# Kernel tuning notes

Hardware: AMD Instinct MI355X
Metric: run time of the kernel (lower is better)

## Reference

```python
import jax, jax.numpy as jnp
import numpy as np

OUT_LEN = 25  # fixed self.out_length
H1, H2, D_IN, D_OUT = 9, 32, 5, 3


def _rnn_last(x_tbd, Wih, Whh, b):
    """Elman tanh RNN, time-major input [T,B,D]; returns final hidden [B,H]."""
    B = x_tbd.shape[1]
    h0 = jnp.zeros((B, Wih.shape[0]), x_tbd.dtype)
    def step(h, x_t):
        h = jnp.tanh(x_t @ Wih.T + h @ Whh.T + b)
        return h, None
    h_last, _ = jax.lax.scan(step, h0, x_tbd)
    return h_last


def _rnn_all(x_tbd, Wih, Whh, b):
    """Elman tanh RNN, time-major input [T,B,D]; returns all hiddens [T,B,H]."""
    B = x_tbd.shape[1]
    h0 = jnp.zeros((B, Wih.shape[0]), x_tbd.dtype)
    def step(h, x_t):
        h = jnp.tanh(x_t @ Wih.T + h @ Whh.T + b)
        return h, h
    _, hs = jax.lax.scan(step, h0, x_tbd)
    return hs


def setup_inputs() -> dict:
    key = jax.random.key(0)
    ks = jax.random.split(key, 16)
    B, T = 4096, 2048
    s1 = 1.0 / np.sqrt(H1)
    s2 = 1.0 / np.sqrt(H2)
    u = lambda k, shp, s: jax.random.uniform(k, shp, jnp.float32, -s, s)
    return {
        "x": jax.random.uniform(ks[0], (B, T, D_IN), jnp.float32),
        # rnn_1 forward direction
        "w_ih_f": u(ks[1], (H1, D_IN), s1), "w_hh_f": u(ks[2], (H1, H1), s1),
        "b_ih_f": u(ks[3], (H1,), s1),     "b_hh_f": u(ks[4], (H1,), s1),
        # rnn_1 backward direction
        "w_ih_b": u(ks[5], (H1, D_IN), s1), "w_hh_b": u(ks[6], (H1, H1), s1),
        "b_ih_b": u(ks[7], (H1,), s1),      "b_hh_b": u(ks[8], (H1,), s1),
        # rnn_2 (input 2*H1=18, hidden 32)
        "w_ih2": u(ks[9], (H2, 2 * H1), s2), "w_hh2": u(ks[10], (H2, H2), s2),
        "b_ih2": u(ks[11], (H2,), s2),       "b_hh2": u(ks[12], (H2,), s2),
        # output linear 32 -> 3
        "w_out": u(ks[13], (D_OUT, H2), s2), "b_out": u(ks[14], (D_OUT,), s2),
    }


def reference(x, w_ih_f, w_hh_f, b_ih_f, b_hh_f,
              w_ih_b, w_hh_b, b_ih_b, b_hh_b,
              w_ih2, w_hh2, b_ih2, b_hh2, w_out, b_out):
    B = x.shape[0]
    xt = jnp.swapaxes(x, 0, 1)  # [T,B,5]
    h_f = _rnn_last(xt, w_ih_f, w_hh_f, b_ih_f + b_hh_f)          # [B,9]
    h_b = _rnn_last(xt[::-1], w_ih_b, w_hh_b, b_ih_b + b_hh_b)    # [B,9]
    y = jnp.concatenate([h_f, h_b], axis=1)                       # [B,18]
    # u: zeros over OUT_LEN steps with y at t=0 (time-major)
    u = jnp.zeros((OUT_LEN, B, 2 * H1), x.dtype).at[0].set(y)
    ys = _rnn_all(u, w_ih2, w_hh2, b_ih2 + b_hh2)                 # [25,B,32]
    ys = jnp.swapaxes(ys, 0, 1)                                   # [B,25,32]
    out = jnp.einsum('bth,oh->bto', ys, w_out) + b_out            # [B,25,3]
    return out
```

## Files before the change

kernel.cpp:

```cpp
#include <hip/hip_runtime.h>

#define RNN_T 2048
#define RNN_B 4096
#define BLK 16
#define NBLK (RNN_T / BLK)
#define CHF (BLK * 5)
#define WVF (4 * CHF)
#define BLF (16 * CHF)

__device__ __forceinline__ void async4(const float* src, float* dst) {
    __builtin_amdgcn_global_load_lds(
        (const __attribute__((address_space(1))) void*)src,
        (__attribute__((address_space(3))) void*)dst, 4, 0, 0);
}

__device__ __forceinline__ void fill_wave(float* dstWave, const float* x,
                                          unsigned (&off)[5], int adv) {
#pragma unroll
    for (int j = 0; j < 5; ++j) {
        async4(x + off[j], dstWave + j * 64);
        off[j] += (unsigned)adv;
    }
}

__device__ __forceinline__ void stepr(float& h, float xn, const float (&W)[16],
                                      float bb, bool own) {
    float a0 = fmaf(h, W[0], bb);
    float a1, a2;
    asm ("s_nop 1\n\t"
         "v_fmac_f32_dpp %0, %3, %4  row_ror:1  row_mask:0xf bank_mask:0xf\n\t"
         "v_mul_f32_dpp  %1, %3, %5  row_ror:2  row_mask:0xf bank_mask:0xf\n\t"
         "v_mul_f32_dpp  %2, %3, %6  row_ror:3  row_mask:0xf bank_mask:0xf\n\t"
         "v_fmac_f32_dpp %0, %3, %7  row_ror:4  row_mask:0xf bank_mask:0xf\n\t"
         "v_fmac_f32_dpp %1, %3, %8  row_ror:5  row_mask:0xf bank_mask:0xf\n\t"
         "v_fmac_f32_dpp %2, %3, %9  row_ror:6  row_mask:0xf bank_mask:0xf\n\t"
         "v_fmac_f32_dpp %0, %3, %10 row_ror:7  row_mask:0xf bank_mask:0xf\n\t"
         "v_fmac_f32_dpp %1, %3, %11 row_ror:8  row_mask:0xf bank_mask:0xf\n\t"
         "v_fmac_f32_dpp %2, %3, %12 row_ror:9  row_mask:0xf bank_mask:0xf\n\t"
         "v_fmac_f32_dpp %0, %3, %13 row_ror:10 row_mask:0xf bank_mask:0xf\n\t"
         "v_fmac_f32_dpp %1, %3, %14 row_ror:11 row_mask:0xf bank_mask:0xf\n\t"
         "v_fmac_f32_dpp %2, %3, %15 row_ror:12 row_mask:0xf bank_mask:0xf\n\t"
         "v_fmac_f32_dpp %0, %3, %16 row_ror:13 row_mask:0xf bank_mask:0xf\n\t"
         "v_fmac_f32_dpp %1, %3, %17 row_ror:14 row_mask:0xf bank_mask:0xf\n\t"
         "v_fmac_f32_dpp %2, %3, %18 row_ror:15 row_mask:0xf bank_mask:0xf"
         : "+v"(a0), "=&v"(a1), "=&v"(a2)
         : "v"(h), "v"(W[1]), "v"(W[2]), "v"(W[3]), "v"(W[4]), "v"(W[5]),
           "v"(W[6]), "v"(W[7]), "v"(W[8]), "v"(W[9]), "v"(W[10]), "v"(W[11]),
           "v"(W[12]), "v"(W[13]), "v"(W[14]), "v"(W[15]));
    const float z = (a0 + a1) + a2;
    const float e = __builtin_amdgcn_exp2f(z);
    const float u = __builtin_amdgcn_rcpf(e + 1.0f);
    h = own ? u : xn;
}

template <bool FWD, bool FILL>
__device__ __forceinline__ void compute_block(const float* xc, const float* xnb,
        float& h, const float (&W)[16], float bb, bool own,
        float* fillDst, const float* x, unsigned (&off)[5], int adv) {
    float xn[16];
#pragma unroll
    for (int j = 0; j < 15; ++j) xn[j] = xc[FWD ? (j + 1) * 5 : (14 - j) * 5];
    xn[15] = xnb[FWD ? 0 : 75];
    if constexpr (FILL) fill_wave(fillDst, x, off, adv);
#pragma unroll
    for (int j = 0; j < 16; ++j) stepr(h, xn[j], W, bb, own);
}

template <bool FWD>
__device__ __forceinline__ float run_all(const float* xcA, const float* xcB,
        const float* xcC, float* wA, float* wB, float* wC,
        const float* x, unsigned (&off)[5], int adv,
        const float (&W)[16], float bb, bool own) {
    fill_wave(wA, x, off, adv);
    fill_wave(wB, x, off, adv);
    float h = own ? 0.5f : xcA[FWD ? 0 : 75];
#pragma unroll 1
    for (int it = 0; it < 42; ++it) {
        compute_block<FWD, true >(xcA, xcB, h, W, bb, own, wC, x, off, adv);
        compute_block<FWD, true >(xcB, xcC, h, W, bb, own, wA, x, off, adv);
        compute_block<FWD, true >(xcC, xcA, h, W, bb, own, wB, x, off, adv);
    }
    compute_block<FWD, false>(xcA, xcB, h, W, bb, own, wC, x, off, adv);
    compute_block<FWD, false>(xcB, xcB, h, W, bb, own, wC, x, off, adv);
    return h;
}

__global__ __launch_bounds__(256, 2) void rnn1_kernel(
    const float* __restrict__ x,
    const float* __restrict__ w_ih_f, const float* __restrict__ w_hh_f,
    const float* __restrict__ b_ih_f, const float* __restrict__ b_hh_f,
    const float* __restrict__ w_ih_b, const float* __restrict__ w_hh_b,
    const float* __restrict__ b_ih_b, const float* __restrict__ b_hh_b,
    float* __restrict__ y)
{
    __shared__ __align__(16) float sA[BLF], sB[BLF], sC[BLF];
    const float SC = 2.8853900817779268f;
    const int tid    = threadIdx.x;
    const int group  = tid >> 4;
    const int lane16 = tid & 15;
    const int waveId = tid >> 6;
    const int lane   = tid & 63;
    const int chain  = blockIdx.x * 16 + group;
    const int b      = chain & (RNN_B - 1);
    const int dir    = chain >> 12;

    const float* __restrict__ wih = dir ? w_ih_b : w_ih_f;
    const float* __restrict__ whh = dir ? w_hh_b : w_hh_f;
    const float* __restrict__ bih = dir ? b_ih_b : b_ih_f;
    const float* __restrict__ bhh = dir ? b_hh_b : b_hh_f;

    const int   li  = (lane16 < 9) ? lane16 : 0;
    const float msk = (lane16 < 9) ? SC : 0.0f;
    const bool  own = (lane16 < 9);
    float W[16];
    float wsum = 0.0f;
#pragma unroll
    for (int r = 0; r < 16; ++r) {
        const int s = (lane16 - r) & 15;
        float w = 0.0f;
        bool hs = false;
        if (s < 9)       { w = whh[li * 9 + s]; hs = true; }
        else if (s < 14) w = wih[li * 5 + (s - 9)];
        w *= msk;
        if (hs) { wsum += w; w *= -2.0f; }
        W[r] = w;
    }
    const float bb = (bih[li] + bhh[li]) * msk + wsum;

    unsigned off[5];
#pragma unroll
    for (int j = 0; j < 5; ++j) {
        const int idx = j * 64 + lane;
        const int gf  = idx / 80;
        const int p   = idx - gf * 80;
        const int bf  = (blockIdx.x * 16 + waveId * 4 + gf) & (RNN_B - 1);
        off[j] = (unsigned)(bf * (RNN_T * 5) + (dir ? (NBLK - 1) * CHF : 0) + p);
    }
    const int adv = dir ? -CHF : CHF;

    float* wA = sA + waveId * WVF;
    float* wB = sB + waveId * WVF;
    float* wC = sC + waveId * WVF;
    const int xoff = own ? 0 : ((lane16 < 14) ? (lane16 - 9) : 0);
    const float* xcA = sA + group * CHF + xoff;
    const float* xcB = sB + group * CHF + xoff;
    const float* xcC = sC + group * CHF + xoff;

    float h = dir ? run_all<false>(xcA, xcB, xcC, wA, wB, wC, x, off, adv, W, bb, own)
                  : run_all<true >(xcA, xcB, xcC, wA, wB, wC, x, off, adv, W, bb, own);

    if (lane16 < 9) y[b * 18 + dir * 9 + lane16] = fmaf(-2.0f, h, 1.0f);
}

__global__ __launch_bounds__(256) void rnn2_kernel(
    const float* __restrict__ y,
    const float* __restrict__ w_ih2, const float* __restrict__ w_hh2,
    const float* __restrict__ b_ih2, const float* __restrict__ b_hh2,
    const float* __restrict__ w_out, const float* __restrict__ b_out,
    float* __restrict__ out)
{
    __shared__ float hist[8][25][32];
    const float SC = 2.8853900817779268f;
    const int bl = threadIdx.x >> 5;
    const int i  = threadIdx.x & 31;
    const int b  = blockIdx.x * 8 + bl;

    float wr[32];
#pragma unroll
    for (int k = 0; k < 32; ++k) wr[k] = w_hh2[i * 32 + k] * SC;
    const float bias = (b_ih2[i] + b_hh2[i]) * SC;

    const float* yb = y + b * 18;
    float z = bias;
#pragma unroll
    for (int k = 0; k < 18; ++k) z = fmaf(w_ih2[i * 18 + k] * SC, yb[k], z);
    {
        float e = __builtin_amdgcn_exp2f(z);
        float r = __builtin_amdgcn_rcpf(e + 1.0f);
        hist[bl][0][i] = fmaf(-2.0f, r, 1.0f);
    }
    __syncthreads();

    for (int t = 1; t < 25; ++t) {
        float zz = bias;
#pragma unroll
        for (int k = 0; k < 32; ++k) zz = fmaf(wr[k], hist[bl][t - 1][k], zz);
        float e = __builtin_amdgcn_exp2f(zz);
        float r = __builtin_amdgcn_rcpf(e + 1.0f);
        hist[bl][t][i] = fmaf(-2.0f, r, 1.0f);
        __syncthreads();
    }

    for (int e = threadIdx.x; e < 600; e += 256) {
        const int o  = e % 3;
        const int t  = (e / 3) % 25;
        const int b2 = e / 75;
        float acc = b_out[o];
#pragma unroll
        for (int k = 0; k < 32; ++k) acc = fmaf(w_out[o * 32 + k], hist[b2][t][k], acc);
        out[((size_t)(blockIdx.x * 8 + b2) * 25 + t) * 3 + o] = acc;
    }
}

extern "C" void kernel_launch(void* const* d_in, const int* in_sizes, int n_in,
                              void* d_out, int out_size, void* d_ws, size_t ws_size,
                              hipStream_t stream) {
    const float* x      = (const float*)d_in[0];
    const float* w_ih_f = (const float*)d_in[1];
    const float* w_hh_f = (const float*)d_in[2];
    const float* b_ih_f = (const float*)d_in[3];
    const float* b_hh_f = (const float*)d_in[4];
    const float* w_ih_b = (const float*)d_in[5];
    const float* w_hh_b = (const float*)d_in[6];
    const float* b_ih_b = (const float*)d_in[7];
    const float* b_hh_b = (const float*)d_in[8];
    const float* w_ih2  = (const float*)d_in[9];
    const float* w_hh2  = (const float*)d_in[10];
    const float* b_ih2  = (const float*)d_in[11];
    const float* b_hh2  = (const float*)d_in[12];
    const float* w_out  = (const float*)d_in[13];
    const float* b_out  = (const float*)d_in[14];

    float* y = (float*)d_ws;

    rnn1_kernel<<<dim3(512), dim3(256), 0, stream>>>(
        x, w_ih_f, w_hh_f, b_ih_f, b_hh_f,
        w_ih_b, w_hh_b, b_ih_b, b_hh_b, y);

    rnn2_kernel<<<dim3(RNN_B / 8), dim3(256), 0, stream>>>(
        y, w_ih2, w_hh2, b_ih2, b_hh2, w_out, b_out, (float*)d_out);
}
```

Measured before the change: 418.1 us.

## Interleave two independent RNN chains per lane group to hide transcendental latency

```diff
diff --git a/kernel.cpp b/kernel.cpp
--- a/kernel.cpp
+++ b/kernel.cpp
@@ -5,8 +5,8 @@
 #define BLK 16
 #define NBLK (RNN_T / BLK)
 #define CHF (BLK * 5)
-#define WVF (4 * CHF)
-#define BLF (16 * CHF)
+#define WVF (8 * CHF)
+#define BLF (32 * CHF)
 
 __device__ __forceinline__ void async4(const float* src, float* dst) {
     __builtin_amdgcn_global_load_lds(
@@ -15,16 +15,16 @@
 }
 
 __device__ __forceinline__ void fill_wave(float* dstWave, const float* x,
-                                          unsigned (&off)[5], int adv) {
-#pragma unroll
-    for (int j = 0; j < 5; ++j) {
+                                          unsigned (&off)[10], int adv) {
+#pragma unroll
+    for (int j = 0; j < 10; ++j) {
         async4(x + off[j], dstWave + j * 64);
         off[j] += (unsigned)adv;
     }
 }
 
-__device__ __forceinline__ void stepr(float& h, float xn, const float (&W)[16],
-                                      float bb, bool own) {
+__device__ __forceinline__ void mac16(float h, const float (&W)[16], float bb,
+                                      float& a0o, float& a1o, float& a2o) {
     float a0 = fmaf(h, W[0], bb);
     float a1, a2;
     asm ("s_nop 1\n\t"
@@ -47,45 +47,62 @@
          : "v"(h), "v"(W[1]), "v"(W[2]), "v"(W[3]), "v"(W[4]), "v"(W[5]),
            "v"(W[6]), "v"(W[7]), "v"(W[8]), "v"(W[9]), "v"(W[10]), "v"(W[11]),
            "v"(W[12]), "v"(W[13]), "v"(W[14]), "v"(W[15]));
-    const float z = (a0 + a1) + a2;
-    const float e = __builtin_amdgcn_exp2f(z);
-    const float u = __builtin_amdgcn_rcpf(e + 1.0f);
-    h = own ? u : xn;
+    a0o = a0; a1o = a1; a2o = a2;
 }
 
 template <bool FWD, bool FILL>
-__device__ __forceinline__ void compute_block(const float* xc, const float* xnb,
-        float& h, const float (&W)[16], float bb, bool own,
-        float* fillDst, const float* x, unsigned (&off)[5], int adv) {
-    float xn[16];
-#pragma unroll
-    for (int j = 0; j < 15; ++j) xn[j] = xc[FWD ? (j + 1) * 5 : (14 - j) * 5];
-    xn[15] = xnb[FWD ? 0 : 75];
+__device__ __forceinline__ void compute_block2(const float* xcA, const float* xcAn,
+        const float* xcB, const float* xcBn,
+        float& hA, float& hB, const float (&W)[16], float bb, bool own,
+        float* fillDst, const float* x, unsigned (&off)[10], int adv) {
+    float xnA[16], xnB[16];
+#pragma unroll
+    for (int j = 0; j < 15; ++j) {
+        xnA[j] = xcA[FWD ? (j + 1) * 5 : (14 - j) * 5];
+        xnB[j] = xcB[FWD ? (j + 1) * 5 : (14 - j) * 5];
+    }
+    xnA[15] = xcAn[FWD ? 0 : 75];
+    xnB[15] = xcBn[FWD ? 0 : 75];
     if constexpr (FILL) fill_wave(fillDst, x, off, adv);
-#pragma unroll
-    for (int j = 0; j < 16; ++j) stepr(h, xn[j], W, bb, own);
+
+    float a0, a1, a2, b0, b1, b2, eA, eB;
+    mac16(hA, W, bb, a0, a1, a2);
+    eA = __builtin_amdgcn_exp2f((a0 + a1) + a2);
+    mac16(hB, W, bb, b0, b1, b2);
+    { float u = __builtin_amdgcn_rcpf(eA + 1.0f); hA = own ? u : xnA[0]; }
+    eB = __builtin_amdgcn_exp2f((b0 + b1) + b2);
+#pragma unroll
+    for (int j = 1; j < 16; ++j) {
+        mac16(hA, W, bb, a0, a1, a2);
+        { float u = __builtin_amdgcn_rcpf(eB + 1.0f); hB = own ? u : xnB[j - 1]; }
+        eA = __builtin_amdgcn_exp2f((a0 + a1) + a2);
+        mac16(hB, W, bb, b0, b1, b2);
+        { float u = __builtin_amdgcn_rcpf(eA + 1.0f); hA = own ? u : xnA[j]; }
+        eB = __builtin_amdgcn_exp2f((b0 + b1) + b2);
+    }
+    { float u = __builtin_amdgcn_rcpf(eB + 1.0f); hB = own ? u : xnB[15]; }
 }
 
 template <bool FWD>
-__device__ __forceinline__ float run_all(const float* xcA, const float* xcB,
-        const float* xcC, float* wA, float* wB, float* wC,
-        const float* x, unsigned (&off)[5], int adv,
-        const float (&W)[16], float bb, bool own) {
+__device__ __forceinline__ void run_all2(const float* pA, const float* pB,
+        const float* pC, float* wA, float* wB, float* wC,
+        const float* x, unsigned (&off)[10], int adv,
+        const float (&W)[16], float bb, bool own, float& hA, float& hB) {
     fill_wave(wA, x, off, adv);
     fill_wave(wB, x, off, adv);
-    float h = own ? 0.5f : xcA[FWD ? 0 : 75];
+    hA = own ? 0.5f : pA[FWD ? 0 : 75];
+    hB = own ? 0.5f : pA[320 + (FWD ? 0 : 75)];
 #pragma unroll 1
     for (int it = 0; it < 42; ++it) {
-        compute_block<FWD, true >(xcA, xcB, h, W, bb, own, wC, x, off, adv);
-        compute_block<FWD, true >(xcB, xcC, h, W, bb, own, wA, x, off, adv);
-        compute_block<FWD, true >(xcC, xcA, h, W, bb, own, wB, x, off, adv);
-    }
-    compute_block<FWD, false>(xcA, xcB, h, W, bb, own, wC, x, off, adv);
-    compute_block<FWD, false>(xcB, xcB, h, W, bb, own, wC, x, off, adv);
-    return h;
-}
-
-__global__ __launch_bounds__(256, 2) void rnn1_kernel(
+        compute_block2<FWD, true >(pA, pB, pA + 320, pB + 320, hA, hB, W, bb, own, wC, x, off, adv);
+        compute_block2<FWD, true >(pB, pC, pB + 320, pC + 320, hA, hB, W, bb, own, wA, x, off, adv);
+        compute_block2<FWD, true >(pC, pA, pC + 320, pA + 320, hA, hB, W, bb, own, wB, x, off, adv);
+    }
+    compute_block2<FWD, false>(pA, pB, pA + 320, pB + 320, hA, hB, W, bb, own, wC, x, off, adv);
+    compute_block2<FWD, false>(pB, pB, pB + 320, pB + 320, hA, hB, W, bb, own, wC, x, off, adv);
+}
+
+__global__ __launch_bounds__(256, 1) void rnn1_kernel(
     const float* __restrict__ x,
     const float* __restrict__ w_ih_f, const float* __restrict__ w_hh_f,
     const float* __restrict__ b_ih_f, const float* __restrict__ b_hh_f,
@@ -100,9 +117,9 @@
     const int lane16 = tid & 15;
     const int waveId = tid >> 6;
     const int lane   = tid & 63;
-    const int chain  = blockIdx.x * 16 + group;
-    const int b      = chain & (RNN_B - 1);
-    const int dir    = chain >> 12;
+    const int slot   = blockIdx.x * 16 + group;
+    const int dir    = (slot >= 2048) ? 1 : 0;
+    const int bA     = slot - (dir ? 2048 : 0);
 
     const float* __restrict__ wih = dir ? w_ih_b : w_ih_f;
     const float* __restrict__ whh = dir ? w_hh_b : w_hh_f;
@@ -127,13 +144,14 @@
     }
     const float bb = (bih[li] + bhh[li]) * msk + wsum;
 
-    unsigned off[5];
-#pragma unroll
-    for (int j = 0; j < 5; ++j) {
+    unsigned off[10];
+#pragma unroll
+    for (int j = 0; j < 10; ++j) {
         const int idx = j * 64 + lane;
         const int gf  = idx / 80;
         const int p   = idx - gf * 80;
-        const int bf  = (blockIdx.x * 16 + waveId * 4 + gf) & (RNN_B - 1);
+        const int slotf = blockIdx.x * 16 + waveId * 4 + (gf & 3);
+        const int bf  = (slotf - (dir ? 2048 : 0)) + ((gf >= 4) ? 2048 : 0);
         off[j] = (unsigned)(bf * (RNN_T * 5) + (dir ? (NBLK - 1) * CHF : 0) + p);
     }
     const int adv = dir ? -CHF : CHF;
@@ -141,15 +159,20 @@
     float* wA = sA + waveId * WVF;
     float* wB = sB + waveId * WVF;
     float* wC = sC + waveId * WVF;
-    const int xoff = own ? 0 : ((lane16 < 14) ? (lane16 - 9) : 0);
-    const float* xcA = sA + group * CHF + xoff;
-    const float* xcB = sB + group * CHF + xoff;
-    const float* xcC = sC + group * CHF + xoff;
-
-    float h = dir ? run_all<false>(xcA, xcB, xcC, wA, wB, wC, x, off, adv, W, bb, own)
-                  : run_all<true >(xcA, xcB, xcC, wA, wB, wC, x, off, adv, W, bb, own);
-
-    if (lane16 < 9) y[b * 18 + dir * 9 + lane16] = fmaf(-2.0f, h, 1.0f);
+    const int xoff  = own ? 0 : ((lane16 < 14) ? (lane16 - 9) : 0);
+    const int gbase = waveId * WVF + (group & 3) * CHF + xoff;
+    const float* pA = sA + gbase;
+    const float* pB = sB + gbase;
+    const float* pC = sC + gbase;
+
+    float hA, hB;
+    if (dir) run_all2<false>(pA, pB, pC, wA, wB, wC, x, off, adv, W, bb, own, hA, hB);
+    else     run_all2<true >(pA, pB, pC, wA, wB, wC, x, off, adv, W, bb, own, hA, hB);
+
+    if (lane16 < 9) {
+        y[bA * 18 + dir * 9 + lane16]          = fmaf(-2.0f, hA, 1.0f);
+        y[(bA + 2048) * 18 + dir * 9 + lane16] = fmaf(-2.0f, hB, 1.0f);
+    }
 }
 
 __global__ __launch_bounds__(256) void rnn2_kernel(
@@ -223,7 +246,7 @@
 
     float* y = (float*)d_ws;
 
-    rnn1_kernel<<<dim3(512), dim3(256), 0, stream>>>(
+    rnn1_kernel<<<dim3(256), dim3(256), 0, stream>>>(
         x, w_ih_f, w_hh_f, b_ih_f, b_hh_f,
         w_ih_b, w_hh_b, b_ih_b, b_hh_b, y);
 
```

New measurement: 482.0 us. +15.3%, slower.

## Double time chunk and transpose LDS staging for vectorized float4 reads

Applied to the files above, without the earlier changes.

```diff
diff --git a/kernel.cpp b/kernel.cpp
--- a/kernel.cpp
+++ b/kernel.cpp
@@ -2,7 +2,7 @@
 
 #define RNN_T 2048
 #define RNN_B 4096
-#define BLK 16
+#define BLK 32
 #define NBLK (RNN_T / BLK)
 #define CHF (BLK * 5)
 #define WVF (4 * CHF)
@@ -15,9 +15,9 @@
 }
 
 __device__ __forceinline__ void fill_wave(float* dstWave, const float* x,
-                                          unsigned (&off)[5], int adv) {
-#pragma unroll
-    for (int j = 0; j < 5; ++j) {
+                                          unsigned (&off)[10], int adv) {
+#pragma unroll
+    for (int j = 0; j < 10; ++j) {
         async4(x + off[j], dstWave + j * 64);
         off[j] += (unsigned)adv;
     }
@@ -54,34 +54,43 @@
 }
 
 template <bool FWD, bool FILL>
-__device__ __forceinline__ void compute_block(const float* xc, const float* xnb,
+__device__ __forceinline__ void compute_block(const float* xc,
         float& h, const float (&W)[16], float bb, bool own,
-        float* fillDst, const float* x, unsigned (&off)[5], int adv) {
-    float xn[16];
-#pragma unroll
-    for (int j = 0; j < 15; ++j) xn[j] = xc[FWD ? (j + 1) * 5 : (14 - j) * 5];
-    xn[15] = xnb[FWD ? 0 : 75];
+        float* fillDst, const float* x, unsigned (&off)[10], int adv) {
+    float xn[32];
+#pragma unroll
+    for (int j = 0; j < 8; ++j) {
+        const float4 v = *reinterpret_cast<const float4*>(xc + j * 4);
+        xn[j * 4 + 0] = v.x; xn[j * 4 + 1] = v.y;
+        xn[j * 4 + 2] = v.z; xn[j * 4 + 3] = v.w;
+    }
+    h = own ? h : xn[FWD ? 0 : 31];
     if constexpr (FILL) fill_wave(fillDst, x, off, adv);
 #pragma unroll
-    for (int j = 0; j < 16; ++j) stepr(h, xn[j], W, bb, own);
+    for (int j = 0; j < 32; ++j) {
+        const int nidx = FWD ? (j < 31 ? j + 1 : 31) : (j < 31 ? 30 - j : 0);
+        stepr(h, xn[nidx], W, bb, own);
+    }
 }
 
 template <bool FWD>
 __device__ __forceinline__ float run_all(const float* xcA, const float* xcB,
         const float* xcC, float* wA, float* wB, float* wC,
-        const float* x, unsigned (&off)[5], int adv,
+        const float* x, unsigned (&off)[10], int adv,
         const float (&W)[16], float bb, bool own) {
     fill_wave(wA, x, off, adv);
     fill_wave(wB, x, off, adv);
-    float h = own ? 0.5f : xcA[FWD ? 0 : 75];
+    float h = own ? 0.5f : 0.0f;
 #pragma unroll 1
-    for (int it = 0; it < 42; ++it) {
-        compute_block<FWD, true >(xcA, xcB, h, W, bb, own, wC, x, off, adv);
-        compute_block<FWD, true >(xcB, xcC, h, W, bb, own, wA, x, off, adv);
-        compute_block<FWD, true >(xcC, xcA, h, W, bb, own, wB, x, off, adv);
-    }
-    compute_block<FWD, false>(xcA, xcB, h, W, bb, own, wC, x, off, adv);
-    compute_block<FWD, false>(xcB, xcB, h, W, bb, own, wC, x, off, adv);
+    for (int it = 0; it < 20; ++it) {
+        compute_block<FWD, true >(xcA, h, W, bb, own, wC, x, off, adv);
+        compute_block<FWD, true >(xcB, h, W, bb, own, wA, x, off, adv);
+        compute_block<FWD, true >(xcC, h, W, bb, own, wB, x, off, adv);
+    }
+    compute_block<FWD, true >(xcA, h, W, bb, own, wC, x, off, adv);
+    compute_block<FWD, true >(xcB, h, W, bb, own, wA, x, off, adv);
+    compute_block<FWD, false>(xcC, h, W, bb, own, wC, x, off, adv);
+    compute_block<FWD, false>(xcA, h, W, bb, own, wC, x, off, adv);
     return h;
 }
 
@@ -127,24 +136,28 @@
     }
     const float bb = (bih[li] + bhh[li]) * msk + wsum;
 
-    unsigned off[5];
-#pragma unroll
-    for (int j = 0; j < 5; ++j) {
+    unsigned off[10];
+#pragma unroll
+    for (int j = 0; j < 10; ++j) {
         const int idx = j * 64 + lane;
-        const int gf  = idx / 80;
-        const int p   = idx - gf * 80;
-        const int bf  = (blockIdx.x * 16 + waveId * 4 + gf) & (RNN_B - 1);
-        off[j] = (unsigned)(bf * (RNN_T * 5) + (dir ? (NBLK - 1) * CHF : 0) + p);
+        const int g   = idx / 160;
+        const int q   = idx - g * 160;
+        const int c   = q / 32;
+        const int t   = q - c * 32;
+        const int bf  = (blockIdx.x * 16 + waveId * 4 + g) & (RNN_B - 1);
+        off[j] = (unsigned)(bf * (RNN_T * 5) + (dir ? (NBLK - 1) * CHF : 0)
+                            + t * 5 + c);
     }
     const int adv = dir ? -CHF : CHF;
 
     float* wA = sA + waveId * WVF;
     float* wB = sB + waveId * WVF;
     float* wC = sC + waveId * WVF;
-    const int xoff = own ? 0 : ((lane16 < 14) ? (lane16 - 9) : 0);
-    const float* xcA = sA + group * CHF + xoff;
-    const float* xcB = sB + group * CHF + xoff;
-    const float* xcC = sC + group * CHF + xoff;
+    const int cbase = own ? 0 : ((lane16 < 14) ? (lane16 - 9) * BLK : 0);
+    const int gbase = waveId * WVF + (group & 3) * CHF + cbase;
+    const float* xcA = sA + gbase;
+    const float* xcB = sB + gbase;
+    const float* xcC = sC + gbase;
 
     float h = dir ? run_all<false>(xcA, xcB, xcC, wA, wB, wC, x, off, adv, W, bb, own)
                   : run_all<true >(xcA, xcB, xcC, wA, wB, wC, x, off, adv, W, bb, own);
```

Result: no change. 424.2 us (+1.4%).
